# Optimization experiments

Measured on AMD Instinct MI355X. Metric: run time of the kernel, lower is better.

## Reference

```python
import jax, jax.numpy as jnp
import numpy as np

B, T, D, H = 4, 2048, 1024, 16
HD = D // H  # head_dim = 64

def setup_inputs() -> dict:
    key = jax.random.key(0)
    k1, k2, k3 = jax.random.split(key, 3)
    scale_in = 1.0 / np.sqrt(D)
    return {
        "x": jax.random.normal(k1, (B, T, D), dtype=jnp.float32),
        "W_qkv": jax.random.normal(k2, (D, 3 * D), dtype=jnp.float32) * scale_in,
        "b_qkv": jnp.zeros((3 * D,), dtype=jnp.float32),
        "W_out": jax.random.normal(k3, (D, D), dtype=jnp.float32) * scale_in,
        "b_out": jnp.zeros((D,), dtype=jnp.float32),
    }

def reference(x, W_qkv, b_qkv, W_out, b_out):
    Bx, Tx, C = x.shape
    qkv = x @ W_qkv + b_qkv                      # [B,T,3D]
    q, k, v = jnp.split(qkv, 3, axis=-1)
    # [B,T,D] -> [B,H,T,hd]
    def to_heads(t):
        return t.reshape(Bx, Tx, H, HD).transpose(0, 2, 1, 3)
    q, k, v = to_heads(q), to_heads(k), to_heads(v)
    scores = jnp.einsum('bhqd,bhkd->bhqk', q, k) / np.sqrt(HD)  # [B,H,T,T]
    causal = jnp.tril(jnp.ones((Tx, Tx), dtype=bool))
    scores = jnp.where(causal, scores, -jnp.inf)
    attn = jax.nn.softmax(scores, axis=-1)       # dropout p=0 -> identity
    out = jnp.einsum('bhqk,bhkd->bhqd', attn, v)  # [B,H,T,hd]
    out = out.transpose(0, 2, 1, 3).reshape(Bx, Tx, C)
    return out @ W_out + b_out
```

## Files before the change

### kernel.cpp

```cpp
#include <hip/hip_runtime.h>
#include <hip/hip_bf16.h>

#define BB 4
#define TT 2048
#define DD 1024
#define HH 16
#define HDIM 64
#define BT (BB*TT)
#define D3 (3*DD)

typedef __attribute__((ext_vector_type(8))) short bf16x8;
typedef __attribute__((ext_vector_type(4))) float f32x4;

#if __has_builtin(__builtin_amdgcn_exp2f)
#define EXP2(x) __builtin_amdgcn_exp2f(x)
#else
#define EXP2(x) exp2f(x)
#endif

__device__ __forceinline__ ushort f2bf(float f) {
  union { float f; uint32_t u; } v; v.f = f;
  uint32_t u = v.u + 0x7FFFu + ((v.u >> 16) & 1u);
  return (ushort)(u >> 16);
}

__device__ __forceinline__ ushort f2bf_hw(float f) {
  __hip_bfloat16 h = __float2bfloat16(f);
  ushort u;
  __builtin_memcpy(&u, &h, 2);
  return u;
}

__device__ __forceinline__ float bf2f(ushort u) {
  union { uint32_t i; float f; } x; x.i = ((uint32_t)u) << 16; return x.f;
}

__device__ __forceinline__ void gload_lds16(const void* g, void* l) {
  __builtin_amdgcn_global_load_lds((const __attribute__((address_space(1))) void*)g,
                                   (__attribute__((address_space(3))) void*)l, 16, 0, 0);
}

__global__ __launch_bounds__(256)
void cvt_bf16(const float* __restrict__ in, ushort* __restrict__ out, int n4) {
  int i = blockIdx.x * blockDim.x + threadIdx.x;
  int stride = gridDim.x * blockDim.x;
  for (; i < n4; i += stride) {
    float4 v = ((const float4*)in)[i];
    ushort4 o;
    o.x = f2bf(v.x); o.y = f2bf(v.y); o.z = f2bf(v.z); o.w = f2bf(v.w);
    ((ushort4*)out)[i] = o;
  }
}

__global__ __launch_bounds__(256)
void transpose_cvt(const float* __restrict__ W, ushort* __restrict__ Wt, int K, int N) {
  __shared__ ushort Tt[64][68];
  const int n0 = blockIdx.x * 64;
  const int k0 = blockIdx.y * 64;
  const int tid = threadIdx.x;
  const int r = tid >> 4;
  const int c4 = (tid & 15) * 4;
  #pragma unroll
  for (int i = 0; i < 4; ++i) {
    int row = r + i * 16;
    float4 v = *(const float4*)&W[(size_t)(k0 + row) * N + n0 + c4];
    Tt[c4 + 0][row] = f2bf(v.x);
    Tt[c4 + 1][row] = f2bf(v.y);
    Tt[c4 + 2][row] = f2bf(v.z);
    Tt[c4 + 3][row] = f2bf(v.w);
  }
  __syncthreads();
  #pragma unroll
  for (int i = 0; i < 4; ++i) {
    int row = r + i * 16;
    ushort4 tv = *(const ushort4*)&Tt[row][c4];
    *(ushort4*)&Wt[(size_t)(n0 + row) * K + k0 + c4] = tv;
  }
}

template<bool F32OUT>
__global__ __launch_bounds__(256)
void gemm_bt(const ushort* __restrict__ A, const ushort* __restrict__ Bw,
             const float* __restrict__ bias, void* __restrict__ C, int N) {
  __shared__ __align__(16) short As[128 * 64];
  __shared__ __align__(16) short Bs[128 * 64];
  const int tid = threadIdx.x;
  const int w = tid >> 6, lane = tid & 63;
  const int li = lane & 15, g = lane >> 4;
  const int wm = w >> 1, wn = w & 1;
  const int bm = blockIdx.y * 128;
  const int bn = blockIdx.x * 128;
  const int lrow = lane >> 3;
  const int lchunk = lane & 7;

  f32x4 acc[4][4] = {};

  for (int k0 = 0; k0 < 1024; k0 += 64) {
    __syncthreads();
    #pragma unroll
    for (int j = 0; j < 4; ++j) {
      int row = j * 32 + w * 8 + lrow;
      gload_lds16(A  + (size_t)(bm + row) * 1024 + k0 + lchunk * 8, As + j * 2048 + w * 512);
      gload_lds16(Bw + (size_t)(bn + row) * 1024 + k0 + lchunk * 8, Bs + j * 2048 + w * 512);
    }
    __syncthreads();
    #pragma unroll
    for (int c = 0; c < 2; ++c) {
      bf16x8 af[4], bfr[4];
      #pragma unroll
      for (int mi = 0; mi < 4; ++mi)
        af[mi] = *(bf16x8*)&As[(wm * 64 + mi * 16 + li) * 64 + c * 32 + g * 8];
      #pragma unroll
      for (int ni = 0; ni < 4; ++ni)
        bfr[ni] = *(bf16x8*)&Bs[(wn * 64 + ni * 16 + li) * 64 + c * 32 + g * 8];
      #pragma unroll
      for (int mi = 0; mi < 4; ++mi)
        #pragma unroll
        for (int ni = 0; ni < 4; ++ni)
          acc[mi][ni] = __builtin_amdgcn_mfma_f32_16x16x32_bf16(af[mi], bfr[ni], acc[mi][ni], 0, 0, 0);
    }
  }
  #pragma unroll
  for (int ni = 0; ni < 4; ++ni) {
    int col = bn + wn * 64 + ni * 16 + li;
    float bv = bias[col];
    #pragma unroll
    for (int mi = 0; mi < 4; ++mi) {
      int row = bm + wm * 64 + mi * 16 + g * 4;
      #pragma unroll
      for (int r = 0; r < 4; ++r) {
        float v = acc[mi][ni][r] + bv;
        if (F32OUT) ((float*)C)[(size_t)(row + r) * N + col] = v;
        else        ((ushort*)C)[(size_t)(row + r) * N + col] = f2bf_hw(v);
      }
    }
  }
}

__global__ __launch_bounds__(256)
void attn_mfma(const ushort* __restrict__ qkv, ushort* __restrict__ out) {
  __shared__ __align__(16) short Ks[64 * 64];
  __shared__ __align__(16) short Vt[64 * 64];
  __shared__ __align__(16) short Pl[4 * 16 * 64];

  const int bx = blockIdx.x;
  const int gi = bx >> 8;
  const int rr = bx & 255;
  const int t  = rr & 15;
  const int bh = gi * 16 + (rr >> 4);
  int qt;
  if      (gi == 0) qt = 15 - t;
  else if (gi == 1) qt = t;
  else if (gi == 2) qt = (7 - t) & 15;
  else              qt = (t + 8) & 15;

  const int h = bh & 15, b = bh >> 4;
  const int tid = threadIdx.x;
  const int w = tid >> 6;
  const int lane = tid & 63;
  const int li = lane & 15, g = lane >> 4;
  const int sw = (li & 7) << 4;

  char* KsB = (char*)Ks;
  char* VtB = (char*)Vt;
  char* PlB = (char*)Pl + w * 2048;

  const int q0 = qt * 128;
  const int qg0 = q0 + w * 32;

  bf16x8 qfr[2][2];
  #pragma unroll
  for (int qf = 0; qf < 2; ++qf) {
    const ushort* qrow = qkv + (size_t)(b * TT + qg0 + qf * 16 + li) * D3 + h * HDIM;
    #pragma unroll
    for (int c = 0; c < 2; ++c) {
      uint4 raw = *(const uint4*)(qrow + c * 32 + g * 8);
      const ushort* rp = (const ushort*)&raw;
      bf16x8 v;
      #pragma unroll
      for (int j = 0; j < 8; ++j)
        v[j] = (short)f2bf_hw(bf2f(rp[j]) * 0.18033688f);
      qfr[qf][c] = v;
    }
  }

  f32x4 o[4][2] = {};
  float lsum[2] = {0.f, 0.f};

  const ushort* kbase = qkv + (size_t)b * TT * D3 + DD + h * HDIM;
  const ushort* vbase = kbase + DD;

  const int krow0 = tid >> 3;
  const int kc = tid & 7;
  const int d0 = (tid >> 5) * 8;
  const int kp = tid & 31;

  const int nt = 2 * qt + 2;
  const int itlast = 2 * qt + (w >> 1);

  uint4 kpre0, kpre1, vpre0, vpre1;
  {
    const ushort* kg = kbase + (size_t)krow0 * D3 + kc * 8;
    kpre0 = *(const uint4*)kg;
    kpre1 = *(const uint4*)(kg + (size_t)32 * D3);
    const ushort* vg = vbase + (size_t)(2 * kp) * D3 + d0;
    vpre0 = *(const uint4*)vg;
    vpre1 = *(const uint4*)(vg + D3);
  }

  const int kswz = (kc * 16) ^ ((krow0 & 7) << 4);

  for (int it = 0; it < nt; ++it) {
    const int k0 = it * 64;
    *(uint4*)(KsB + krow0 * 128 + kswz) = kpre0;
    *(uint4*)(KsB + (krow0 + 32) * 128 + kswz) = kpre1;
    {
      const ushort* pa = (const ushort*)&vpre0;
      const ushort* pb = (const ushort*)&vpre1;
      #pragma unroll
      for (int j = 0; j < 8; ++j) {
        uint32_t pk = (uint32_t)pa[j] | ((uint32_t)pb[j] << 16);
        *(uint32_t*)(VtB + (d0 + j) * 128 + ((4 * kp) ^ (j << 4))) = pk;
      }
    }
    __syncthreads();
    if (it + 1 < nt) {
      const ushort* kg = kbase + (size_t)(k0 + 64 + krow0) * D3 + kc * 8;
      kpre0 = *(const uint4*)kg;
      kpre1 = *(const uint4*)(kg + (size_t)32 * D3);
      const ushort* vg = vbase + (size_t)(k0 + 64 + 2 * kp) * D3 + d0;
      vpre0 = *(const uint4*)vg;
      vpre1 = *(const uint4*)(vg + D3);
    }
    if (it <= itlast) {
      const bool domask = (it == itlast);
      bf16x8 pf[2][2];
      f32x4 s[2][4];
      __builtin_amdgcn_s_setprio(1);
      #pragma unroll
      for (int kt = 0; kt < 4; ++kt) {
        const int row = kt * 16 + li;
        bf16x8 kf0 = *(bf16x8*)(KsB + row * 128 + ((g * 16) ^ sw));
        bf16x8 kf1 = *(bf16x8*)(KsB + row * 128 + ((64 + g * 16) ^ sw));
        #pragma unroll
        for (int qf = 0; qf < 2; ++qf) {
          f32x4 a = {0.f, 0.f, 0.f, 0.f};
          a = __builtin_amdgcn_mfma_f32_16x16x32_bf16(kf0, qfr[qf][0], a, 0, 0, 0);
          a = __builtin_amdgcn_mfma_f32_16x16x32_bf16(kf1, qfr[qf][1], a, 0, 0, 0);
          s[qf][kt] = a;
        }
      }
      __builtin_amdgcn_s_setprio(0);
      #pragma unroll
      for (int qf = 0; qf < 2; ++qf) {
        const int qrow = qg0 + qf * 16 + li;
        if (domask) {
          #pragma unroll
          for (int kt = 0; kt < 4; ++kt)
            #pragma unroll
            for (int r = 0; r < 4; ++r) {
              int key = k0 + kt * 16 + g * 4 + r;
              if (key > qrow) s[qf][kt][r] = -1e30f;
            }
        }
        float ls = 0.f;
        #pragma unroll
        for (int kt = 0; kt < 4; ++kt) {
          float p0 = EXP2(s[qf][kt][0]);
          float p1 = EXP2(s[qf][kt][1]);
          float p2 = EXP2(s[qf][kt][2]);
          float p3 = EXP2(s[qf][kt][3]);
          ls += (p0 + p1) + (p2 + p3);
          uint2 val;
          val.x = (uint32_t)f2bf_hw(p0) | ((uint32_t)f2bf_hw(p1) << 16);
          val.y = (uint32_t)f2bf_hw(p2) | ((uint32_t)f2bf_hw(p3) << 16);
          *(uint2*)(PlB + li * 128 + ((kt * 32 + g * 8) ^ sw)) = val;
        }
        lsum[qf] += ls;
        pf[qf][0] = *(bf16x8*)(PlB + li * 128 + ((g * 16) ^ sw));
        pf[qf][1] = *(bf16x8*)(PlB + li * 128 + ((64 + g * 16) ^ sw));
      }
      __builtin_amdgcn_s_setprio(1);
      #pragma unroll
      for (int dt = 0; dt < 4; ++dt) {
        const int vrow = dt * 16 + li;
        bf16x8 vf0 = *(bf16x8*)(VtB + vrow * 128 + ((g * 16) ^ sw));
        bf16x8 vf1 = *(bf16x8*)(VtB + vrow * 128 + ((64 + g * 16) ^ sw));
        #pragma unroll
        for (int qf = 0; qf < 2; ++qf) {
          o[dt][qf] = __builtin_amdgcn_mfma_f32_16x16x32_bf16(vf0, pf[qf][0], o[dt][qf], 0, 0, 0);
          o[dt][qf] = __builtin_amdgcn_mfma_f32_16x16x32_bf16(vf1, pf[qf][1], o[dt][qf], 0, 0, 0);
        }
      }
      __builtin_amdgcn_s_setprio(0);
    }
    __syncthreads();
  }

  #pragma unroll
  for (int qf = 0; qf < 2; ++qf) {
    float lt = lsum[qf];
    lt += __shfl_xor(lt, 16);
    lt += __shfl_xor(lt, 32);
    float inv = 1.f / lt;
    ushort* orow = out + (size_t)(b * TT + qg0 + qf * 16 + li) * DD + h * HDIM;
    #pragma unroll
    for (int dt = 0; dt < 4; ++dt) {
      uint2 pk;
      pk.x = (uint32_t)f2bf_hw(o[dt][qf][0] * inv) | ((uint32_t)f2bf_hw(o[dt][qf][1] * inv) << 16);
      pk.y = (uint32_t)f2bf_hw(o[dt][qf][2] * inv) | ((uint32_t)f2bf_hw(o[dt][qf][3] * inv) << 16);
      *(uint2*)&orow[dt * 16 + g * 4] = pk;
    }
  }
}

extern "C" void kernel_launch(void* const* d_in, const int* in_sizes, int n_in,
                              void* d_out, int out_size, void* d_ws, size_t ws_size,
                              hipStream_t stream) {
  const float* x     = (const float*)d_in[0];
  const float* W_qkv = (const float*)d_in[1];
  const float* b_qkv = (const float*)d_in[2];
  const float* W_out = (const float*)d_in[3];
  const float* b_out = (const float*)d_in[4];
  float* out = (float*)d_out;

  ushort* x_bf   = (ushort*)d_ws;
  ushort* wtq    = x_bf + (size_t)BT * DD;
  ushort* wto    = wtq + (size_t)D3 * DD;
  ushort* qkv_bf = wto + (size_t)DD * DD;
  ushort* att_bf = qkv_bf + (size_t)BT * D3;

  cvt_bf16<<<2048, 256, 0, stream>>>(x, x_bf, BT * DD / 4);
  transpose_cvt<<<dim3(D3 / 64, DD / 64), 256, 0, stream>>>(W_qkv, wtq, DD, D3);
  transpose_cvt<<<dim3(DD / 64, DD / 64), 256, 0, stream>>>(W_out, wto, DD, DD);

  gemm_bt<false><<<dim3(D3 / 128, BT / 128), 256, 0, stream>>>(x_bf, wtq, b_qkv, (void*)qkv_bf, D3);
  attn_mfma<<<dim3(64 * (TT / 128)), 256, 0, stream>>>(qkv_bf, att_bf);
  gemm_bt<true><<<dim3(DD / 128, BT / 128), 256, 0, stream>>>(att_bf, wto, b_out, (void*)out, DD);
}
```

Before: 204.0 us.

## Schedule attention tiles dynamically via atomic work counter, longest-first

Replaces the static blockIdx-to-(query tile, head) mapping in the attention kernel with an atomic counter that hands out work items. Items are ordered so the longest causal query tiles are issued first. Blocks loop, grabbing items until the counter runs past the total. The aim is better load balance across CUs given the triangular causal work. It adds a counter-reset kernel and one global atomic plus a block barrier per item.

```diff
diff --git a/kernel.cpp b/kernel.cpp
--- a/kernel.cpp
+++ b/kernel.cpp
@@ -137,24 +137,18 @@
   }
 }
 
+__global__ void zero_ctr(uint* c) { *c = 0u; }
+
+#define NITEMS 1024
+
 __global__ __launch_bounds__(256)
-void attn_mfma(const ushort* __restrict__ qkv, ushort* __restrict__ out) {
+void attn_mfma(const ushort* __restrict__ qkv, ushort* __restrict__ out,
+               uint* __restrict__ ctr) {
   __shared__ __align__(16) short Ks[64 * 64];
   __shared__ __align__(16) short Vt[64 * 64];
   __shared__ __align__(16) short Pl[4 * 16 * 64];
-
-  const int bx = blockIdx.x;
-  const int gi = bx >> 8;
-  const int rr = bx & 255;
-  const int t  = rr & 15;
-  const int bh = gi * 16 + (rr >> 4);
-  int qt;
-  if      (gi == 0) qt = 15 - t;
-  else if (gi == 1) qt = t;
-  else if (gi == 2) qt = (7 - t) & 15;
-  else              qt = (t + 8) & 15;
-
-  const int h = bh & 15, b = bh >> 4;
+  __shared__ int s_item;
+
   const int tid = threadIdx.x;
   const int w = tid >> 6;
   const int lane = tid & 63;
@@ -165,151 +159,159 @@
   char* VtB = (char*)Vt;
   char* PlB = (char*)Pl + w * 2048;
 
-  const int q0 = qt * 128;
-  const int qg0 = q0 + w * 32;
-
-  bf16x8 qfr[2][2];
-  #pragma unroll
-  for (int qf = 0; qf < 2; ++qf) {
-    const ushort* qrow = qkv + (size_t)(b * TT + qg0 + qf * 16 + li) * D3 + h * HDIM;
-    #pragma unroll
-    for (int c = 0; c < 2; ++c) {
-      uint4 raw = *(const uint4*)(qrow + c * 32 + g * 8);
-      const ushort* rp = (const ushort*)&raw;
-      bf16x8 v;
-      #pragma unroll
-      for (int j = 0; j < 8; ++j)
-        v[j] = (short)f2bf_hw(bf2f(rp[j]) * 0.18033688f);
-      qfr[qf][c] = v;
-    }
-  }
-
-  f32x4 o[4][2] = {};
-  float lsum[2] = {0.f, 0.f};
-
-  const ushort* kbase = qkv + (size_t)b * TT * D3 + DD + h * HDIM;
-  const ushort* vbase = kbase + DD;
-
   const int krow0 = tid >> 3;
   const int kc = tid & 7;
   const int d0 = (tid >> 5) * 8;
   const int kp = tid & 31;
-
-  const int nt = 2 * qt + 2;
-  const int itlast = 2 * qt + (w >> 1);
-
-  uint4 kpre0, kpre1, vpre0, vpre1;
-  {
-    const ushort* kg = kbase + (size_t)krow0 * D3 + kc * 8;
-    kpre0 = *(const uint4*)kg;
-    kpre1 = *(const uint4*)(kg + (size_t)32 * D3);
-    const ushort* vg = vbase + (size_t)(2 * kp) * D3 + d0;
-    vpre0 = *(const uint4*)vg;
-    vpre1 = *(const uint4*)(vg + D3);
-  }
-
   const int kswz = (kc * 16) ^ ((krow0 & 7) << 4);
 
-  for (int it = 0; it < nt; ++it) {
-    const int k0 = it * 64;
-    *(uint4*)(KsB + krow0 * 128 + kswz) = kpre0;
-    *(uint4*)(KsB + (krow0 + 32) * 128 + kswz) = kpre1;
+  for (;;) {
+    if (tid == 0) s_item = (int)atomicAdd(ctr, 1u);
+    __syncthreads();
+    const int item = s_item;
+    if (item >= NITEMS) return;
+
+    const int qt = 15 - (item >> 6);
+    const int bh = item & 63;
+    const int h = bh & 15, b = bh >> 4;
+    const int qg0 = qt * 128 + w * 32;
+
+    bf16x8 qfr[2][2];
+    #pragma unroll
+    for (int qf = 0; qf < 2; ++qf) {
+      const ushort* qrow = qkv + (size_t)(b * TT + qg0 + qf * 16 + li) * D3 + h * HDIM;
+      #pragma unroll
+      for (int c = 0; c < 2; ++c) {
+        uint4 raw = *(const uint4*)(qrow + c * 32 + g * 8);
+        const ushort* rp = (const ushort*)&raw;
+        bf16x8 v;
+        #pragma unroll
+        for (int j = 0; j < 8; ++j)
+          v[j] = (short)f2bf_hw(bf2f(rp[j]) * 0.18033688f);
+        qfr[qf][c] = v;
+      }
+    }
+
+    f32x4 o[4][2] = {};
+    float lsum[2] = {0.f, 0.f};
+
+    const ushort* kbase = qkv + (size_t)b * TT * D3 + DD + h * HDIM;
+    const ushort* vbase = kbase + DD;
+
+    const int nt = 2 * qt + 2;
+    const int itlast = 2 * qt + (w >> 1);
+
+    uint4 kpre0, kpre1, vpre0, vpre1;
     {
-      const ushort* pa = (const ushort*)&vpre0;
-      const ushort* pb = (const ushort*)&vpre1;
-      #pragma unroll
-      for (int j = 0; j < 8; ++j) {
-        uint32_t pk = (uint32_t)pa[j] | ((uint32_t)pb[j] << 16);
-        *(uint32_t*)(VtB + (d0 + j) * 128 + ((4 * kp) ^ (j << 4))) = pk;
-      }
-    }
-    __syncthreads();
-    if (it + 1 < nt) {
-      const ushort* kg = kbase + (size_t)(k0 + 64 + krow0) * D3 + kc * 8;
+      const ushort* kg = kbase + (size_t)krow0 * D3 + kc * 8;
       kpre0 = *(const uint4*)kg;
       kpre1 = *(const uint4*)(kg + (size_t)32 * D3);
-      const ushort* vg = vbase + (size_t)(k0 + 64 + 2 * kp) * D3 + d0;
+      const ushort* vg = vbase + (size_t)(2 * kp) * D3 + d0;
       vpre0 = *(const uint4*)vg;
       vpre1 = *(const uint4*)(vg + D3);
     }
-    if (it <= itlast) {
-      const bool domask = (it == itlast);
-      bf16x8 pf[2][2];
-      f32x4 s[2][4];
-      __builtin_amdgcn_s_setprio(1);
-      #pragma unroll
-      for (int kt = 0; kt < 4; ++kt) {
-        const int row = kt * 16 + li;
-        bf16x8 kf0 = *(bf16x8*)(KsB + row * 128 + ((g * 16) ^ sw));
-        bf16x8 kf1 = *(bf16x8*)(KsB + row * 128 + ((64 + g * 16) ^ sw));
+
+    for (int it = 0; it < nt; ++it) {
+      const int k0 = it * 64;
+      *(uint4*)(KsB + krow0 * 128 + kswz) = kpre0;
+      *(uint4*)(KsB + (krow0 + 32) * 128 + kswz) = kpre1;
+      {
+        const ushort* pa = (const ushort*)&vpre0;
+        const ushort* pb = (const ushort*)&vpre1;
+        #pragma unroll
+        for (int j = 0; j < 8; ++j) {
+          uint32_t pk = (uint32_t)pa[j] | ((uint32_t)pb[j] << 16);
+          *(uint32_t*)(VtB + (d0 + j) * 128 + ((4 * kp) ^ (j << 4))) = pk;
+        }
+      }
+      __syncthreads();
+      if (it + 1 < nt) {
+        const ushort* kg = kbase + (size_t)(k0 + 64 + krow0) * D3 + kc * 8;
+        kpre0 = *(const uint4*)kg;
+        kpre1 = *(const uint4*)(kg + (size_t)32 * D3);
+        const ushort* vg = vbase + (size_t)(k0 + 64 + 2 * kp) * D3 + d0;
+        vpre0 = *(const uint4*)vg;
+        vpre1 = *(const uint4*)(vg + D3);
+      }
+      if (it <= itlast) {
+        const bool domask = (it == itlast);
+        bf16x8 pf[2][2];
+        f32x4 s[2][4];
+        __builtin_amdgcn_s_setprio(1);
+        #pragma unroll
+        for (int kt = 0; kt < 4; ++kt) {
+          const int row = kt * 16 + li;
+          bf16x8 kf0 = *(bf16x8*)(KsB + row * 128 + ((g * 16) ^ sw));
+          bf16x8 kf1 = *(bf16x8*)(KsB + row * 128 + ((64 + g * 16) ^ sw));
+          #pragma unroll
+          for (int qf = 0; qf < 2; ++qf) {
+            f32x4 a = {0.f, 0.f, 0.f, 0.f};
+            a = __builtin_amdgcn_mfma_f32_16x16x32_bf16(kf0, qfr[qf][0], a, 0, 0, 0);
+            a = __builtin_amdgcn_mfma_f32_16x16x32_bf16(kf1, qfr[qf][1], a, 0, 0, 0);
+            s[qf][kt] = a;
+          }
+        }
+        __builtin_amdgcn_s_setprio(0);
         #pragma unroll
         for (int qf = 0; qf < 2; ++qf) {
-          f32x4 a = {0.f, 0.f, 0.f, 0.f};
-          a = __builtin_amdgcn_mfma_f32_16x16x32_bf16(kf0, qfr[qf][0], a, 0, 0, 0);
-          a = __builtin_amdgcn_mfma_f32_16x16x32_bf16(kf1, qfr[qf][1], a, 0, 0, 0);
-          s[qf][kt] = a;
+          const int qrow = qg0 + qf * 16 + li;
+          if (domask) {
+            #pragma unroll
+            for (int kt = 0; kt < 4; ++kt)
+              #pragma unroll
+              for (int r = 0; r < 4; ++r) {
+                int key = k0 + kt * 16 + g * 4 + r;
+                if (key > qrow) s[qf][kt][r] = -1e30f;
+              }
+          }
+          float ls = 0.f;
+          #pragma unroll
+          for (int kt = 0; kt < 4; ++kt) {
+            float p0 = EXP2(s[qf][kt][0]);
+            float p1 = EXP2(s[qf][kt][1]);
+            float p2 = EXP2(s[qf][kt][2]);
+            float p3 = EXP2(s[qf][kt][3]);
+            ls += (p0 + p1) + (p2 + p3);
+            uint2 val;
+            val.x = (uint32_t)f2bf_hw(p0) | ((uint32_t)f2bf_hw(p1) << 16);
+            val.y = (uint32_t)f2bf_hw(p2) | ((uint32_t)f2bf_hw(p3) << 16);
+            *(uint2*)(PlB + li * 128 + ((kt * 32 + g * 8) ^ sw)) = val;
+          }
+          lsum[qf] += ls;
+          pf[qf][0] = *(bf16x8*)(PlB + li * 128 + ((g * 16) ^ sw));
+          pf[qf][1] = *(bf16x8*)(PlB + li * 128 + ((64 + g * 16) ^ sw));
         }
-      }
-      __builtin_amdgcn_s_setprio(0);
-      #pragma unroll
-      for (int qf = 0; qf < 2; ++qf) {
-        const int qrow = qg0 + qf * 16 + li;
-        if (domask) {
+        __builtin_amdgcn_s_setprio(1);
+        #pragma unroll
+        for (int dt = 0; dt < 4; ++dt) {
+          const int vrow = dt * 16 + li;
+          bf16x8 vf0 = *(bf16x8*)(VtB + vrow * 128 + ((g * 16) ^ sw));
+          bf16x8 vf1 = *(bf16x8*)(VtB + vrow * 128 + ((64 + g * 16) ^ sw));
           #pragma unroll
-          for (int kt = 0; kt < 4; ++kt)
-            #pragma unroll
-            for (int r = 0; r < 4; ++r) {
-              int key = k0 + kt * 16 + g * 4 + r;
-              if (key > qrow) s[qf][kt][r] = -1e30f;
-            }
+          for (int qf = 0; qf < 2; ++qf) {
+            o[dt][qf] = __builtin_amdgcn_mfma_f32_16x16x32_bf16(vf0, pf[qf][0], o[dt][qf], 0, 0, 0);
+            o[dt][qf] = __builtin_amdgcn_mfma_f32_16x16x32_bf16(vf1, pf[qf][1], o[dt][qf], 0, 0, 0);
+          }
         }
-        float ls = 0.f;
-        #pragma unroll
-        for (int kt = 0; kt < 4; ++kt) {
-          float p0 = EXP2(s[qf][kt][0]);
-          float p1 = EXP2(s[qf][kt][1]);
-          float p2 = EXP2(s[qf][kt][2]);
-          float p3 = EXP2(s[qf][kt][3]);
-          ls += (p0 + p1) + (p2 + p3);
-          uint2 val;
-          val.x = (uint32_t)f2bf_hw(p0) | ((uint32_t)f2bf_hw(p1) << 16);
-          val.y = (uint32_t)f2bf_hw(p2) | ((uint32_t)f2bf_hw(p3) << 16);
-          *(uint2*)(PlB + li * 128 + ((kt * 32 + g * 8) ^ sw)) = val;
-        }
-        lsum[qf] += ls;
-        pf[qf][0] = *(bf16x8*)(PlB + li * 128 + ((g * 16) ^ sw));
-        pf[qf][1] = *(bf16x8*)(PlB + li * 128 + ((64 + g * 16) ^ sw));
-      }
-      __builtin_amdgcn_s_setprio(1);
+        __builtin_amdgcn_s_setprio(0);
+      }
+      __syncthreads();
+    }
+
+    #pragma unroll
+    for (int qf = 0; qf < 2; ++qf) {
+      float lt = lsum[qf];
+      lt += __shfl_xor(lt, 16);
+      lt += __shfl_xor(lt, 32);
+      float inv = 1.f / lt;
+      ushort* orow = out + (size_t)(b * TT + qg0 + qf * 16 + li) * DD + h * HDIM;
       #pragma unroll
       for (int dt = 0; dt < 4; ++dt) {
-        const int vrow = dt * 16 + li;
-        bf16x8 vf0 = *(bf16x8*)(VtB + vrow * 128 + ((g * 16) ^ sw));
-        bf16x8 vf1 = *(bf16x8*)(VtB + vrow * 128 + ((64 + g * 16) ^ sw));
-        #pragma unroll
-        for (int qf = 0; qf < 2; ++qf) {
-          o[dt][qf] = __builtin_amdgcn_mfma_f32_16x16x32_bf16(vf0, pf[qf][0], o[dt][qf], 0, 0, 0);
-          o[dt][qf] = __builtin_amdgcn_mfma_f32_16x16x32_bf16(vf1, pf[qf][1], o[dt][qf], 0, 0, 0);
-        }
-      }
-      __builtin_amdgcn_s_setprio(0);
-    }
-    __syncthreads();
-  }
-
-  #pragma unroll
-  for (int qf = 0; qf < 2; ++qf) {
-    float lt = lsum[qf];
-    lt += __shfl_xor(lt, 16);
-    lt += __shfl_xor(lt, 32);
-    float inv = 1.f / lt;
-    ushort* orow = out + (size_t)(b * TT + qg0 + qf * 16 + li) * DD + h * HDIM;
-    #pragma unroll
-    for (int dt = 0; dt < 4; ++dt) {
-      uint2 pk;
-      pk.x = (uint32_t)f2bf_hw(o[dt][qf][0] * inv) | ((uint32_t)f2bf_hw(o[dt][qf][1] * inv) << 16);
-      pk.y = (uint32_t)f2bf_hw(o[dt][qf][2] * inv) | ((uint32_t)f2bf_hw(o[dt][qf][3] * inv) << 16);
-      *(uint2*)&orow[dt * 16 + g * 4] = pk;
+        uint2 pk;
+        pk.x = (uint32_t)f2bf_hw(o[dt][qf][0] * inv) | ((uint32_t)f2bf_hw(o[dt][qf][1] * inv) << 16);
+        pk.y = (uint32_t)f2bf_hw(o[dt][qf][2] * inv) | ((uint32_t)f2bf_hw(o[dt][qf][3] * inv) << 16);
+        *(uint2*)&orow[dt * 16 + g * 4] = pk;
+      }
     }
   }
 }
@@ -329,12 +331,14 @@
   ushort* wto    = wtq + (size_t)D3 * DD;
   ushort* qkv_bf = wto + (size_t)DD * DD;
   ushort* att_bf = qkv_bf + (size_t)BT * D3;
-
+  uint*   ctr    = (uint*)(att_bf + (size_t)BT * DD);
+
+  zero_ctr<<<1, 1, 0, stream>>>(ctr);
   cvt_bf16<<<2048, 256, 0, stream>>>(x, x_bf, BT * DD / 4);
   transpose_cvt<<<dim3(D3 / 64, DD / 64), 256, 0, stream>>>(W_qkv, wtq, DD, D3);
   transpose_cvt<<<dim3(DD / 64, DD / 64), 256, 0, stream>>>(W_out, wto, DD, DD);
 
   gemm_bt<false><<<dim3(D3 / 128, BT / 128), 256, 0, stream>>>(x_bf, wtq, b_qkv, (void*)qkv_bf, D3);
-  attn_mfma<<<dim3(64 * (TT / 128)), 256, 0, stream>>>(qkv_bf, att_bf);
+  attn_mfma<<<dim3(1024), 256, 0, stream>>>(qkv_bf, att_bf, ctr);
   gemm_bt<true><<<dim3(DD / 128, BT / 128), 256, 0, stream>>>(att_bf, wto, b_out, (void*)out, DD);
 }
```

New measurement: 201.1 us. About the same (-1.4%).
